# Performance work log

Measured on AMD Instinct MI355X. Metric: run time of the kernel, lower is better.

Reference implementation:

```python
import jax, jax.numpy as jnp
import numpy as np


def setup_inputs() -> dict:
    key = jax.random.key(0)
    ks = jax.random.split(key, 9)
    B, S, D, E, I = 4, 2048, 1024, 8, 2048
    sd = 1.0 / np.sqrt(D)
    si = 1.0 / np.sqrt(I)
    return {
        "hidden_states": jax.random.normal(ks[0], (B, S, D), dtype=jnp.float32),
        "gate_w": jax.random.normal(ks[1], (D, E), dtype=jnp.float32) * sd,
        "expert_gate_w": jax.random.normal(ks[2], (E, D, I), dtype=jnp.float32) * sd,
        "expert_up_w": jax.random.normal(ks[3], (E, D, I), dtype=jnp.float32) * sd,
        "expert_down_w": jax.random.normal(ks[4], (E, I, D), dtype=jnp.float32) * si,
        "shared_gate_proj_w": jax.random.normal(ks[5], (D, I), dtype=jnp.float32) * sd,
        "shared_up_w": jax.random.normal(ks[6], (D, I), dtype=jnp.float32) * sd,
        "shared_down_w": jax.random.normal(ks[7], (I, D), dtype=jnp.float32) * si,
        "shared_expert_gate_w": jax.random.normal(ks[8], (D, 1), dtype=jnp.float32) * sd,
        "top_k": 2,
    }


def reference(hidden_states, gate_w, expert_gate_w, expert_up_w, expert_down_w,
              shared_gate_proj_w, shared_up_w, shared_down_w, shared_expert_gate_w,
              top_k):
    B, S, D = hidden_states.shape
    E = gate_w.shape[1]
    x = hidden_states.reshape(-1, D)            # [T, D]
    T = x.shape[0]

    # Router: softmax in fp32, top-k, dense per-token per-expert combine weights.
    gate_vals = x @ gate_w                      # [T, E]
    probs = jax.nn.softmax(gate_vals.astype(jnp.float32), axis=-1)
    top_w, top_i = jax.lax.top_k(probs, top_k)  # [T, K]
    dense_w = jnp.zeros((T, E), dtype=jnp.float32)
    dense_w = dense_w.at[jnp.arange(T)[:, None], top_i].set(top_w)
    dense_w = dense_w.astype(x.dtype)           # zero for unselected experts

    # All experts as batched SwiGLU GEMMs (tokens with zero weight contribute 0).
    g = jnp.einsum('td,edi->eti', x, expert_gate_w)
    u = jnp.einsum('td,edi->eti', x, expert_up_w)
    y = jnp.einsum('eti,eid->etd', jax.nn.silu(g) * u, expert_down_w)  # [E, T, D]
    moe_out = jnp.einsum('etd,te->td', y, dense_w)                      # [T, D]

    # Shared expert with sigmoid gate.
    shared = (jax.nn.silu(x @ shared_gate_proj_w) * (x @ shared_up_w)) @ shared_down_w
    shared = jax.nn.sigmoid(x @ shared_expert_gate_w) * shared

    final = (moe_out + shared).reshape(B, S, D)
    return final, gate_vals
```

## Files before the change

### kernel.cpp

```cpp
#include <hip/hip_runtime.h>

typedef __bf16 bf16x8 __attribute__((ext_vector_type(8)));
typedef float f32x4 __attribute__((ext_vector_type(4)));
typedef float f4 __attribute__((ext_vector_type(4)));
typedef unsigned short us8 __attribute__((ext_vector_type(8)));

#define T_TOK 8192
#define DDIM 1024
#define NEXP 8
#define IDIM 2048
#define RROWS 17408
#define ROWS_TOT (T_TOK + RROWS)

__device__ __forceinline__ unsigned short f2bf(float f) {
    unsigned u = __float_as_uint(f);
    u += 0x7fffu + ((u >> 16) & 1u);
    return (unsigned short)(u >> 16);
}

__global__ __launch_bounds__(256) void router_kernel(
    const float* __restrict__ x, const float* __restrict__ gate_w,
    const float* __restrict__ sgw, float* __restrict__ gate_out,
    float* __restrict__ wdense, float* __restrict__ sgout)
{
    __shared__ float lgw[DDIM * NEXP];
    __shared__ float lsg[DDIM];
    int tid = threadIdx.x;
    for (int i = tid; i < (DDIM * NEXP) / 4; i += 256)
        ((f4*)lgw)[i] = ((const f4*)gate_w)[i];
    for (int i = tid; i < DDIM / 4; i += 256)
        ((f4*)lsg)[i] = ((const f4*)sgw)[i];
    __syncthreads();

    int wid = tid >> 6, l = tid & 63;
    int t = blockIdx.x * 4 + wid;

    float acc[NEXP];
#pragma unroll
    for (int e = 0; e < NEXP; e++) acc[e] = 0.f;
    float accs = 0.f;
    const float* xr = x + (size_t)t * DDIM;
#pragma unroll
    for (int j = 0; j < 4; j++) {
        int d0 = j * 256 + l * 4;
        f4 xv = *(const f4*)(xr + d0);
#pragma unroll
        for (int c = 0; c < 4; c++) {
            float xd = xv[c];
            int d = d0 + c;
#pragma unroll
            for (int e = 0; e < NEXP; e++) acc[e] += xd * lgw[d * NEXP + e];
            accs += xd * lsg[d];
        }
    }
#pragma unroll
    for (int off = 32; off > 0; off >>= 1) {
#pragma unroll
        for (int e = 0; e < NEXP; e++) acc[e] += __shfl_xor(acc[e], off);
        accs += __shfl_xor(accs, off);
    }
    if (l == 0) {
        float m = acc[0];
        for (int e = 1; e < NEXP; e++) m = fmaxf(m, acc[e]);
        float p[NEXP], s = 0.f;
        for (int e = 0; e < NEXP; e++) { p[e] = __expf(acc[e] - m); s += p[e]; }
        float inv = 1.f / s;
        int i1 = 0; float b1 = p[0];
        for (int e = 1; e < NEXP; e++) if (p[e] > b1) { b1 = p[e]; i1 = e; }
        int i2 = -1; float b2 = -1.f;
        for (int e = 0; e < NEXP; e++) if (e != i1 && p[e] > b2) { b2 = p[e]; i2 = e; }
        for (int e = 0; e < NEXP; e++) {
            gate_out[(size_t)t * NEXP + e] = acc[e];
            float w = (e == i1) ? b1 * inv : (e == i2) ? b2 * inv : 0.f;
            wdense[(size_t)t * NEXP + e] = w;
        }
        sgout[t] = 1.f / (1.f + __expf(-accs));
    }
}

__global__ __launch_bounds__(256) void bucket_kernel(
    const float* __restrict__ wdense, int* __restrict__ list,
    float* __restrict__ wl, int* __restrict__ cnt,
    int* __restrict__ te, int* __restrict__ tp, float* __restrict__ tw)
{
    int e = blockIdx.x;
    int tid = threadIdx.x, wid = tid >> 6, l = tid & 63;
    __shared__ int wsum[4];
    int base = 0;
    int* le = list + (size_t)e * T_TOK;
    float* we = wl + (size_t)e * T_TOK;
    for (int t0 = 0; t0 < T_TOK; t0 += 256) {
        int tok = t0 + tid;
        float w = wdense[(size_t)tok * NEXP + e];
        bool f = w > 0.f;
        unsigned long long m = __ballot(f);
        int lp = __popcll(m & ((1ull << l) - 1ull));
        if (l == 0) wsum[wid] = __popcll(m);
        __syncthreads();
        int woff = 0;
#pragma unroll
        for (int i = 0; i < 4; i++) if (i < wid) woff += wsum[i];
        int btot = wsum[0] + wsum[1] + wsum[2] + wsum[3];
        if (f) {
            int pos = base + woff + lp;
            le[pos] = tok; we[pos] = w;
            int slot = 0;
            for (int e2 = 0; e2 < e; e2++)
                slot += (wdense[(size_t)tok * NEXP + e2] > 0.f) ? 1 : 0;
            te[tok * 2 + slot] = e;
            tp[tok * 2 + slot] = pos;
            tw[tok * 2 + slot] = w;
        }
        base += btot;
        __syncthreads();
    }
    if (tid == 0) cnt[e] = base;
    int align = (base + 127) & ~127;
    for (int i = base + tid; i < align; i += 256) { le[i] = 0; we[i] = 0.f; }
}

__global__ void scan_kernel(const int* __restrict__ cnt, int* __restrict__ offs)
{
    if (threadIdx.x == 0) {
        int o = 0;
        for (int e = 0; e < NEXP; e++) { offs[e] = o; o += (cnt[e] + 127) & ~127; }
    }
}

__global__ __launch_bounds__(256) void cvt_kernel(
    const float* __restrict__ in, unsigned short* __restrict__ out, int n8)
{
    int i = blockIdx.x * 256 + threadIdx.x;
    if (i >= n8) return;
    const f4* p = (const f4*)in + (size_t)i * 2;
    f4 a = p[0], b = p[1];
    us8 o;
#pragma unroll
    for (int k = 0; k < 4; k++) { o[k] = f2bf(a[k]); o[4 + k] = f2bf(b[k]); }
    *((us8*)out + i) = o;
}

__global__ __launch_bounds__(256) void zero_kernel(float* __restrict__ p, int n4)
{
    int i = blockIdx.x * 256 + threadIdx.x;
    if (i < n4) ((f4*)p)[i] = f4{0.f, 0.f, 0.f, 0.f};
}

__global__ __launch_bounds__(256) void wcvt_gu_kernel(
    const float* __restrict__ egw, const float* __restrict__ euw,
    const float* __restrict__ sgp, const float* __restrict__ sup,
    unsigned short* __restrict__ pool, int c0, int NC)
{
    int j = blockIdx.y;
    int e = j >> 1, s = j & 1;
    const float* src = (e < 8) ? ((s ? euw : egw) + (size_t)e * DDIM * IDIM)
                               : (s ? sup : sgp);
    unsigned short* dst = pool + (size_t)j * NC * DDIM;
    int tpc = NC / 64;
    int tci = blockIdx.x % tpc, tri = blockIdx.x / tpc;
    int r0 = tri * 64;
    int cl0 = tci * 64;
    int cg0 = c0 + cl0;

    __shared__ unsigned short lds[64][72];
    int t = threadIdx.x;
    int tr = t >> 4, tcc = (t & 15) * 4;
#pragma unroll
    for (int jj = 0; jj < 4; jj++) {
        int r = tr + jj * 16;
        f4 v = *(const f4*)(src + (size_t)(r0 + r) * IDIM + cg0 + tcc);
#pragma unroll
        for (int k = 0; k < 4; k++) lds[r][tcc + k] = f2bf(v[k]);
    }
    __syncthreads();
    int orow = t >> 2, ss = t & 3;
    us8 v0, v1;
#pragma unroll
    for (int i = 0; i < 8; i++) {
        v0[i] = lds[ss * 16 + i][orow];
        v1[i] = lds[ss * 16 + 8 + i][orow];
    }
    unsigned short* op = dst + (size_t)(cl0 + orow) * DDIM + r0 + ss * 16;
    *(us8*)op = v0; *(us8*)(op + 8) = v1;
}

__global__ __launch_bounds__(256) void wcvt_d_kernel(
    const float* __restrict__ edw, const float* __restrict__ sdw,
    unsigned short* __restrict__ pool, int c0, int NC)
{
    int j = blockIdx.y;
    const float* src = (j < 8) ? edw + (size_t)j * IDIM * DDIM : sdw;
    unsigned short* dst = pool + (size_t)j * DDIM * NC;
    int tpc = DDIM / 64;
    int tci = blockIdx.x % tpc, tri = blockIdx.x / tpc;
    int rl0 = tri * 64;
    int rg0 = c0 + rl0;
    int cg0 = tci * 64;

    __shared__ unsigned short lds[64][72];
    int t = threadIdx.x;
    int tr = t >> 4, tcc = (t & 15) * 4;
#pragma unroll
    for (int jj = 0; jj < 4; jj++) {
        int r = tr + jj * 16;
        f4 v = *(const f4*)(src + (size_t)(rg0 + r) * DDIM + cg0 + tcc);
#pragma unroll
        for (int k = 0; k < 4; k++) lds[r][tcc + k] = f2bf(v[k]);
    }
    __syncthreads();
    int orow = t >> 2, ss = t & 3;
    us8 v0, v1;
#pragma unroll
    for (int i = 0; i < 8; i++) {
        v0[i] = lds[ss * 16 + i][orow];
        v1[i] = lds[ss * 16 + 8 + i][orow];
    }
    unsigned short* op = dst + (size_t)(cg0 + orow) * NC + rl0 + ss * 16;
    *(us8*)op = v0; *(us8*)(op + 8) = v1;
}

__device__ __forceinline__ void stage_tile(
    const unsigned short* __restrict__ g, int row0, int ldk, int k0,
    unsigned short* lds, int wid, int lane)
{
#pragma unroll
    for (int j = 0; j < 2; j++) {
        int c = wid + j * 4;
        int seg = c * 64 + lane;
        int row = seg >> 2, ks = seg & 3;
        const unsigned short* gp = g + (size_t)(row0 + row) * ldk + k0 + ks * 8;
        __builtin_amdgcn_global_load_lds(
            (const __attribute__((address_space(1))) void*)gp,
            (__attribute__((address_space(3))) void*)(lds + c * 512),
            16, 0, 0);
    }
}

__global__ __launch_bounds__(256, 2) void gemm_gateup(
    const unsigned short* __restrict__ A, const unsigned short* __restrict__ pool,
    unsigned short* __restrict__ H, const int* __restrict__ listb,
    const int* __restrict__ cnt, const int* __restrict__ offs, int NC)
{
    int z = blockIdx.z;
    const unsigned short *Bg, *Bu; const int* lst; int count, rowb;
    if (z == 0) {
        Bg = pool + (size_t)16 * NC * DDIM; Bu = pool + (size_t)17 * NC * DDIM;
        lst = nullptr; count = T_TOK; rowb = 0;
    } else {
        int e = z - 1;
        Bg = pool + (size_t)(e * 2) * NC * DDIM; Bu = pool + (size_t)(e * 2 + 1) * NC * DDIM;
        lst = listb + (size_t)e * T_TOK; count = cnt[e]; rowb = T_TOK + offs[e];
    }
    const int K = DDIM;
    int m0 = blockIdx.y * 128, n0 = blockIdx.x * 128;
    if (m0 >= count) return;

    __shared__ unsigned short As[128 * 32], Bgs[128 * 32], Bus[128 * 32];
    int tid = threadIdx.x, wid = tid >> 6, l = tid & 63;
    int wm = wid >> 1, wn = wid & 1;
    int lr = l & 15, kg = l >> 4;

    int seg0 = wid * 64 + l, seg1 = (wid + 4) * 64 + l;
    int ra0 = seg0 >> 2, ka0 = seg0 & 3;
    int ra1 = seg1 >> 2, ka1 = seg1 & 3;
    int ga0 = lst ? lst[m0 + ra0] : (m0 + ra0);
    int ga1 = lst ? lst[m0 + ra1] : (m0 + ra1);
    const unsigned short* pa0 = A + (size_t)ga0 * K + ka0 * 8;
    const unsigned short* pa1 = A + (size_t)ga1 * K + ka1 * 8;

    f32x4 zero = {0.f, 0.f, 0.f, 0.f};
    f32x4 accg[4][4], accu[4][4];
#pragma unroll
    for (int m = 0; m < 4; m++)
#pragma unroll
        for (int n = 0; n < 4; n++) { accg[m][n] = zero; accu[m][n] = zero; }

    for (int k0 = 0; k0 < K; k0 += 32) {
        __builtin_amdgcn_global_load_lds(
            (const __attribute__((address_space(1))) void*)(pa0 + k0),
            (__attribute__((address_space(3))) void*)(As + wid * 512), 16, 0, 0);
        __builtin_amdgcn_global_load_lds(
            (const __attribute__((address_space(1))) void*)(pa1 + k0),
            (__attribute__((address_space(3))) void*)(As + (wid + 4) * 512), 16, 0, 0);
        stage_tile(Bg, n0, K, k0, Bgs, wid, l);
        stage_tile(Bu, n0, K, k0, Bus, wid, l);
        __syncthreads();
        bf16x8 a[4], bg[4], bu[4];
#pragma unroll
        for (int m = 0; m < 4; m++)
            a[m] = *(const bf16x8*)(As + ((wm * 64 + m * 16 + lr) * 32 + kg * 8));
#pragma unroll
        for (int n = 0; n < 4; n++) {
            bg[n] = *(const bf16x8*)(Bgs + ((wn * 64 + n * 16 + lr) * 32 + kg * 8));
            bu[n] = *(const bf16x8*)(Bus + ((wn * 64 + n * 16 + lr) * 32 + kg * 8));
        }
#pragma unroll
        for (int m = 0; m < 4; m++)
#pragma unroll
            for (int n = 0; n < 4; n++) {
                accg[m][n] = __builtin_amdgcn_mfma_f32_16x16x32_bf16(a[m], bg[n], accg[m][n], 0, 0, 0);
                accu[m][n] = __builtin_amdgcn_mfma_f32_16x16x32_bf16(a[m], bu[n], accu[m][n], 0, 0, 0);
            }
        __syncthreads();
    }

#pragma unroll
    for (int m = 0; m < 4; m++) {
        int row = rowb + m0 + wm * 64 + m * 16 + kg * 4;
#pragma unroll
        for (int n = 0; n < 4; n++) {
            int col = n0 + wn * 64 + n * 16 + lr;
#pragma unroll
            for (int r = 0; r < 4; r++) {
                float g = accg[m][n][r], u = accu[m][n][r];
                float hv = g * (1.f / (1.f + __expf(-g))) * u;
                H[(size_t)(row + r) * NC + col] = f2bf(hv);
            }
        }
    }
}

template<int MODE>
__global__ __launch_bounds__(256, 2) void gemm_down(
    const unsigned short* __restrict__ H, const unsigned short* __restrict__ pool,
    float* __restrict__ Y, float* __restrict__ out0,
    const float* __restrict__ wlb, const float* __restrict__ sgo,
    const int* __restrict__ listb, const int* __restrict__ cnt,
    const int* __restrict__ offs, int NC)
{
    int z = blockIdx.z;
    const unsigned short* B; const int* lst; const float* coef; int count, rowb;
    if (z == 0) {
        B = pool + (size_t)8 * DDIM * NC;
        lst = nullptr; coef = sgo; count = T_TOK; rowb = 0;
    } else {
        int e = z - 1;
        B = pool + (size_t)e * DDIM * NC;
        lst = listb + (size_t)e * T_TOK; coef = wlb + (size_t)e * T_TOK;
        count = cnt[e]; rowb = T_TOK + offs[e];
    }
    int m0 = blockIdx.y * 128, n0 = blockIdx.x * 128;
    if (m0 >= count) return;
    const unsigned short* Arows = H + (size_t)rowb * NC;

    __shared__ unsigned short As[128 * 32], Bs[128 * 32];
    int tid = threadIdx.x, wid = tid >> 6, l = tid & 63;
    int wm = wid >> 1, wn = wid & 1;
    int lr = l & 15, kg = l >> 4;

    f32x4 zero = {0.f, 0.f, 0.f, 0.f};
    f32x4 acc[4][4];
#pragma unroll
    for (int m = 0; m < 4; m++)
#pragma unroll
        for (int n = 0; n < 4; n++) acc[m][n] = zero;

    for (int k0 = 0; k0 < NC; k0 += 32) {
        stage_tile(Arows, m0, NC, k0, As, wid, l);
        stage_tile(B, n0, NC, k0, Bs, wid, l);
        __syncthreads();
        bf16x8 a[4], b[4];
#pragma unroll
        for (int m = 0; m < 4; m++)
            a[m] = *(const bf16x8*)(As + ((wm * 64 + m * 16 + lr) * 32 + kg * 8));
#pragma unroll
        for (int n = 0; n < 4; n++)
            b[n] = *(const bf16x8*)(Bs + ((wn * 64 + n * 16 + lr) * 32 + kg * 8));
#pragma unroll
        for (int m = 0; m < 4; m++)
#pragma unroll
            for (int n = 0; n < 4; n++)
                acc[m][n] = __builtin_amdgcn_mfma_f32_16x16x32_bf16(a[m], b[n], acc[m][n], 0, 0, 0);
        __syncthreads();
    }

#pragma unroll
    for (int m = 0; m < 4; m++) {
        int rloc = m0 + wm * 64 + m * 16 + kg * 4;
#pragma unroll
        for (int n = 0; n < 4; n++) {
            int col = n0 + wn * 64 + n * 16 + lr;
#pragma unroll
            for (int r = 0; r < 4; r++) {
                float v = acc[m][n][r];
                if (MODE == 0) {
                    Y[(size_t)(rowb + rloc + r) * DDIM + col] = v;
                } else if (MODE == 1) {
                    Y[(size_t)(rowb + rloc + r) * DDIM + col] += v;
                } else {
                    int rc = rloc + r;
                    if (rc < count) {
                        int tok = lst ? lst[rc] : rc;
                        atomicAdd(&out0[(size_t)tok * DDIM + col], coef[rc] * v);
                    }
                }
            }
        }
    }
}

__global__ __launch_bounds__(256) void combine_kernel(
    const float* __restrict__ Y, const float* __restrict__ sgo,
    const int* __restrict__ te, const int* __restrict__ tp,
    const float* __restrict__ tw, const int* __restrict__ offs,
    float* __restrict__ out)
{
    int t = blockIdx.x * 2 + (threadIdx.x >> 7);
    int c = (threadIdx.x & 127) * 8;
    int e0 = te[2 * t], e1 = te[2 * t + 1];
    size_t r0 = (size_t)T_TOK + offs[e0] + tp[2 * t];
    size_t r1 = (size_t)T_TOK + offs[e1] + tp[2 * t + 1];
    float w0 = tw[2 * t], w1 = tw[2 * t + 1], sg = sgo[t];

    const float* ys = Y + (size_t)t * DDIM + c;
    const float* y0 = Y + r0 * DDIM + c;
    const float* y1 = Y + r1 * DDIM + c;
    f4 s0 = *(const f4*)ys, s1 = *(const f4*)(ys + 4);
    f4 a0 = *(const f4*)y0, a1 = *(const f4*)(y0 + 4);
    f4 b0 = *(const f4*)y1, b1 = *(const f4*)(y1 + 4);
    f4 o0, o1;
#pragma unroll
    for (int k = 0; k < 4; k++) {
        o0[k] = sg * s0[k] + w0 * a0[k] + w1 * b0[k];
        o1[k] = sg * s1[k] + w0 * a1[k] + w1 * b1[k];
    }
    float* op = out + (size_t)t * DDIM + c;
    *(f4*)op = o0;
    *(f4*)(op + 4) = o1;
}

extern "C" void kernel_launch(void* const* d_in, const int* in_sizes, int n_in,
                              void* d_out, int out_size, void* d_ws, size_t ws_size,
                              hipStream_t stream)
{
    const float* x   = (const float*)d_in[0];
    const float* gw  = (const float*)d_in[1];
    const float* egw = (const float*)d_in[2];
    const float* euw = (const float*)d_in[3];
    const float* edw = (const float*)d_in[4];
    const float* sgp = (const float*)d_in[5];
    const float* sup = (const float*)d_in[6];
    const float* sdw = (const float*)d_in[7];
    const float* seg = (const float*)d_in[8];

    float* out0 = (float*)d_out;
    float* gate_out = out0 + (size_t)T_TOK * DDIM;

    auto al = [](size_t b) { return (b + 255) & ~(size_t)255; };
    size_t fixed_b = al((size_t)T_TOK * DDIM * 2)
                   + al((size_t)T_TOK * NEXP * 4)
                   + al((size_t)T_TOK * 4)
                   + al((size_t)NEXP * T_TOK * 4)
                   + al((size_t)NEXP * T_TOK * 4)
                   + 256 + 256
                   + 3 * al((size_t)T_TOK * 2 * 4);
    auto pool_b = [&](int NC) { return al((size_t)18 * NC * DDIM * 2); };
    auto h_b    = [&](int NC) { return al((size_t)ROWS_TOT * NC * 2); };
    size_t y_b  = al((size_t)ROWS_TOT * DDIM * 4);

    int ISPLIT; bool ymode;
    if (fixed_b + pool_b(1024) + h_b(1024) + y_b <= ws_size)      { ISPLIT = 2; ymode = true;  }
    else if (fixed_b + pool_b(1024) + h_b(1024) <= ws_size)       { ISPLIT = 2; ymode = false; }
    else if (fixed_b + pool_b(512) + h_b(512) <= ws_size)         { ISPLIT = 4; ymode = false; }
    else                                                          { ISPLIT = 8; ymode = false; }
    int NC = IDIM / ISPLIT;

    char* ws = (char*)d_ws;
    auto take = [&](size_t bytes) { char* p = ws; ws += (bytes + 255) & ~(size_t)255; return p; };
    unsigned short* xb   = (unsigned short*)take((size_t)T_TOK * DDIM * 2);
    float* wdense = (float*)take((size_t)T_TOK * NEXP * 4);
    float* sgo    = (float*)take((size_t)T_TOK * 4);
    int*   list   = (int*)take((size_t)NEXP * T_TOK * 4);
    float* wl     = (float*)take((size_t)NEXP * T_TOK * 4);
    int*   cnt    = (int*)take(0); ws += 256;
    int*   offs   = (int*)take(0); ws += 256;
    int*   te     = (int*)take((size_t)T_TOK * 2 * 4);
    int*   tp     = (int*)take((size_t)T_TOK * 2 * 4);
    float* tw     = (float*)take((size_t)T_TOK * 2 * 4);
    unsigned short* pool = (unsigned short*)take((size_t)18 * NC * DDIM * 2);
    unsigned short* H    = (unsigned short*)take((size_t)ROWS_TOT * NC * 2);
    float* Y = ymode ? (float*)take((size_t)ROWS_TOT * DDIM * 4) : nullptr;

    router_kernel<<<T_TOK / 4, 256, 0, stream>>>(x, gw, seg, gate_out, wdense, sgo);
    bucket_kernel<<<NEXP, 256, 0, stream>>>(wdense, list, wl, cnt, te, tp, tw);
    scan_kernel<<<1, 64, 0, stream>>>(cnt, offs);
    cvt_kernel<<<(T_TOK * DDIM / 8) / 256, 256, 0, stream>>>(x, xb, T_TOK * DDIM / 8);
    if (!ymode)
        zero_kernel<<<(T_TOK * DDIM / 4) / 256, 256, 0, stream>>>(out0, T_TOK * DDIM / 4);

    for (int c = 0; c < ISPLIT; c++) {
        int c0 = c * NC;
        wcvt_gu_kernel<<<dim3((NC / 64) * 16, 18), 256, 0, stream>>>(
            egw, euw, sgp, sup, pool, c0, NC);
        gemm_gateup<<<dim3(NC / 128, T_TOK / 128, 9), 256, 0, stream>>>(
            xb, pool, H, list, cnt, offs, NC);
        wcvt_d_kernel<<<dim3((NC / 64) * 16, 9), 256, 0, stream>>>(
            edw, sdw, pool, c0, NC);
        if (ymode) {
            if (c == 0)
                gemm_down<0><<<dim3(DDIM / 128, T_TOK / 128, 9), 256, 0, stream>>>(
                    H, pool, Y, out0, wl, sgo, list, cnt, offs, NC);
            else
                gemm_down<1><<<dim3(DDIM / 128, T_TOK / 128, 9), 256, 0, stream>>>(
                    H, pool, Y, out0, wl, sgo, list, cnt, offs, NC);
        } else {
            gemm_down<2><<<dim3(DDIM / 128, T_TOK / 128, 9), 256, 0, stream>>>(
                H, pool, Y, out0, wl, sgo, list, cnt, offs, NC);
        }
    }
    if (ymode)
        combine_kernel<<<T_TOK / 2, 256, 0, stream>>>(Y, sgo, te, tp, tw, offs, out0);
}
```

Before: 632.6 us.

## Run down-projection once over full K with bf16 pre-scaled Y and simplified combine

Restructures the schedule so the gate/up GEMM runs in two column chunks writing into a full-width H buffer, then a single down-projection GEMM runs over the full intermediate dimension. This removes the second down pass and the fp32 Y read-modify-write. The down GEMM folds the routing or shared-gate coefficient into its epilogue and stores Y as bf16. The combine then only sums three bf16 rows. The workspace-dependent fallback paths (atomics, zeroing) are dropped, which assumes the workspace is large enough and adds bf16 rounding on the partial outputs.

```diff
diff --git a/kernel.cpp b/kernel.cpp
--- a/kernel.cpp
+++ b/kernel.cpp
@@ -9,6 +9,7 @@
 #define DDIM 1024
 #define NEXP 8
 #define IDIM 2048
+#define NCH 1024
 #define RROWS 17408
 #define ROWS_TOT (T_TOK + RROWS)
 
@@ -81,7 +82,7 @@
 __global__ __launch_bounds__(256) void bucket_kernel(
     const float* __restrict__ wdense, int* __restrict__ list,
     float* __restrict__ wl, int* __restrict__ cnt,
-    int* __restrict__ te, int* __restrict__ tp, float* __restrict__ tw)
+    int* __restrict__ te, int* __restrict__ tp)
 {
     int e = blockIdx.x;
     int tid = threadIdx.x, wid = tid >> 6, l = tid & 63;
@@ -109,7 +110,6 @@
                 slot += (wdense[(size_t)tok * NEXP + e2] > 0.f) ? 1 : 0;
             te[tok * 2 + slot] = e;
             tp[tok * 2 + slot] = pos;
-            tw[tok * 2 + slot] = w;
         }
         base += btot;
         __syncthreads();
@@ -140,23 +140,17 @@
     *((us8*)out + i) = o;
 }
 
-__global__ __launch_bounds__(256) void zero_kernel(float* __restrict__ p, int n4)
-{
-    int i = blockIdx.x * 256 + threadIdx.x;
-    if (i < n4) ((f4*)p)[i] = f4{0.f, 0.f, 0.f, 0.f};
-}
-
 __global__ __launch_bounds__(256) void wcvt_gu_kernel(
     const float* __restrict__ egw, const float* __restrict__ euw,
     const float* __restrict__ sgp, const float* __restrict__ sup,
-    unsigned short* __restrict__ pool, int c0, int NC)
+    unsigned short* __restrict__ pool, int c0)
 {
     int j = blockIdx.y;
     int e = j >> 1, s = j & 1;
     const float* src = (e < 8) ? ((s ? euw : egw) + (size_t)e * DDIM * IDIM)
                                : (s ? sup : sgp);
-    unsigned short* dst = pool + (size_t)j * NC * DDIM;
-    int tpc = NC / 64;
+    unsigned short* dst = pool + (size_t)j * NCH * DDIM;
+    int tpc = NCH / 64;
     int tci = blockIdx.x % tpc, tri = blockIdx.x / tpc;
     int r0 = tri * 64;
     int cl0 = tci * 64;
@@ -186,15 +180,14 @@
 
 __global__ __launch_bounds__(256) void wcvt_d_kernel(
     const float* __restrict__ edw, const float* __restrict__ sdw,
-    unsigned short* __restrict__ pool, int c0, int NC)
+    unsigned short* __restrict__ pool)
 {
     int j = blockIdx.y;
     const float* src = (j < 8) ? edw + (size_t)j * IDIM * DDIM : sdw;
-    unsigned short* dst = pool + (size_t)j * DDIM * NC;
+    unsigned short* dst = pool + (size_t)j * DDIM * IDIM;
     int tpc = DDIM / 64;
     int tci = blockIdx.x % tpc, tri = blockIdx.x / tpc;
-    int rl0 = tri * 64;
-    int rg0 = c0 + rl0;
+    int rg0 = tri * 64;
     int cg0 = tci * 64;
 
     __shared__ unsigned short lds[64][72];
@@ -215,7 +208,7 @@
         v0[i] = lds[ss * 16 + i][orow];
         v1[i] = lds[ss * 16 + 8 + i][orow];
     }
-    unsigned short* op = dst + (size_t)(cg0 + orow) * NC + rl0 + ss * 16;
+    unsigned short* op = dst + (size_t)(cg0 + orow) * IDIM + rg0 + ss * 16;
     *(us8*)op = v0; *(us8*)(op + 8) = v1;
 }
 
@@ -239,21 +232,23 @@
 __global__ __launch_bounds__(256, 2) void gemm_gateup(
     const unsigned short* __restrict__ A, const unsigned short* __restrict__ pool,
     unsigned short* __restrict__ H, const int* __restrict__ listb,
-    const int* __restrict__ cnt, const int* __restrict__ offs, int NC)
+    const int* __restrict__ cnt, const int* __restrict__ offs, int c0)
 {
     int z = blockIdx.z;
     const unsigned short *Bg, *Bu; const int* lst; int count, rowb;
     if (z == 0) {
-        Bg = pool + (size_t)16 * NC * DDIM; Bu = pool + (size_t)17 * NC * DDIM;
+        Bg = pool + (size_t)16 * NCH * DDIM; Bu = pool + (size_t)17 * NCH * DDIM;
         lst = nullptr; count = T_TOK; rowb = 0;
     } else {
         int e = z - 1;
-        Bg = pool + (size_t)(e * 2) * NC * DDIM; Bu = pool + (size_t)(e * 2 + 1) * NC * DDIM;
+        Bg = pool + (size_t)(e * 2) * NCH * DDIM; Bu = pool + (size_t)(e * 2 + 1) * NCH * DDIM;
         lst = listb + (size_t)e * T_TOK; count = cnt[e]; rowb = T_TOK + offs[e];
     }
+    int flat = blockIdx.y * 8 + blockIdx.x;
+    int nt = flat & 7, mt = flat >> 3;
+    int m0 = mt * 128, n0 = nt * 128;
+    if (m0 >= count) return;
     const int K = DDIM;
-    int m0 = blockIdx.y * 128, n0 = blockIdx.x * 128;
-    if (m0 >= count) return;
 
     __shared__ unsigned short As[128 * 32], Bgs[128 * 32], Bus[128 * 32];
     int tid = threadIdx.x, wid = tid >> 6, l = tid & 63;
@@ -309,39 +304,39 @@
         int row = rowb + m0 + wm * 64 + m * 16 + kg * 4;
 #pragma unroll
         for (int n = 0; n < 4; n++) {
-            int col = n0 + wn * 64 + n * 16 + lr;
+            int col = c0 + n0 + wn * 64 + n * 16 + lr;
 #pragma unroll
             for (int r = 0; r < 4; r++) {
                 float g = accg[m][n][r], u = accu[m][n][r];
                 float hv = g * (1.f / (1.f + __expf(-g))) * u;
-                H[(size_t)(row + r) * NC + col] = f2bf(hv);
+                H[(size_t)(row + r) * IDIM + col] = f2bf(hv);
             }
         }
     }
 }
 
-template<int MODE>
 __global__ __launch_bounds__(256, 2) void gemm_down(
     const unsigned short* __restrict__ H, const unsigned short* __restrict__ pool,
-    float* __restrict__ Y, float* __restrict__ out0,
+    unsigned short* __restrict__ Y,
     const float* __restrict__ wlb, const float* __restrict__ sgo,
-    const int* __restrict__ listb, const int* __restrict__ cnt,
-    const int* __restrict__ offs, int NC)
+    const int* __restrict__ cnt, const int* __restrict__ offs)
 {
     int z = blockIdx.z;
-    const unsigned short* B; const int* lst; const float* coef; int count, rowb;
+    const unsigned short* B; const float* coef; int count, rowb;
     if (z == 0) {
-        B = pool + (size_t)8 * DDIM * NC;
-        lst = nullptr; coef = sgo; count = T_TOK; rowb = 0;
+        B = pool + (size_t)8 * DDIM * IDIM;
+        coef = sgo; count = T_TOK; rowb = 0;
     } else {
         int e = z - 1;
-        B = pool + (size_t)e * DDIM * NC;
-        lst = listb + (size_t)e * T_TOK; coef = wlb + (size_t)e * T_TOK;
+        B = pool + (size_t)e * DDIM * IDIM;
+        coef = wlb + (size_t)e * T_TOK;
         count = cnt[e]; rowb = T_TOK + offs[e];
     }
-    int m0 = blockIdx.y * 128, n0 = blockIdx.x * 128;
+    int flat = blockIdx.y * 8 + blockIdx.x;
+    int nt = flat & 7, mt = flat >> 3;
+    int m0 = mt * 128, n0 = nt * 128;
     if (m0 >= count) return;
-    const unsigned short* Arows = H + (size_t)rowb * NC;
+    const unsigned short* Arows = H + (size_t)rowb * IDIM;
 
     __shared__ unsigned short As[128 * 32], Bs[128 * 32];
     int tid = threadIdx.x, wid = tid >> 6, l = tid & 63;
@@ -355,9 +350,9 @@
 #pragma unroll
         for (int n = 0; n < 4; n++) acc[m][n] = zero;
 
-    for (int k0 = 0; k0 < NC; k0 += 32) {
-        stage_tile(Arows, m0, NC, k0, As, wid, l);
-        stage_tile(B, n0, NC, k0, Bs, wid, l);
+    for (int k0 = 0; k0 < IDIM; k0 += 32) {
+        stage_tile(Arows, m0, IDIM, k0, As, wid, l);
+        stage_tile(B, n0, IDIM, k0, Bs, wid, l);
         __syncthreads();
         bf16x8 a[4], b[4];
 #pragma unroll
@@ -377,32 +372,22 @@
 #pragma unroll
     for (int m = 0; m < 4; m++) {
         int rloc = m0 + wm * 64 + m * 16 + kg * 4;
+        float cf[4];
+#pragma unroll
+        for (int r = 0; r < 4; r++) cf[r] = coef[rloc + r];
 #pragma unroll
         for (int n = 0; n < 4; n++) {
             int col = n0 + wn * 64 + n * 16 + lr;
 #pragma unroll
-            for (int r = 0; r < 4; r++) {
-                float v = acc[m][n][r];
-                if (MODE == 0) {
-                    Y[(size_t)(rowb + rloc + r) * DDIM + col] = v;
-                } else if (MODE == 1) {
-                    Y[(size_t)(rowb + rloc + r) * DDIM + col] += v;
-                } else {
-                    int rc = rloc + r;
-                    if (rc < count) {
-                        int tok = lst ? lst[rc] : rc;
-                        atomicAdd(&out0[(size_t)tok * DDIM + col], coef[rc] * v);
-                    }
-                }
-            }
+            for (int r = 0; r < 4; r++)
+                Y[(size_t)(rowb + rloc + r) * DDIM + col] = f2bf(cf[r] * acc[m][n][r]);
         }
     }
 }
 
 __global__ __launch_bounds__(256) void combine_kernel(
-    const float* __restrict__ Y, const float* __restrict__ sgo,
-    const int* __restrict__ te, const int* __restrict__ tp,
-    const float* __restrict__ tw, const int* __restrict__ offs,
+    const unsigned short* __restrict__ Y, const int* __restrict__ te,
+    const int* __restrict__ tp, const int* __restrict__ offs,
     float* __restrict__ out)
 {
     int t = blockIdx.x * 2 + (threadIdx.x >> 7);
@@ -410,19 +395,19 @@
     int e0 = te[2 * t], e1 = te[2 * t + 1];
     size_t r0 = (size_t)T_TOK + offs[e0] + tp[2 * t];
     size_t r1 = (size_t)T_TOK + offs[e1] + tp[2 * t + 1];
-    float w0 = tw[2 * t], w1 = tw[2 * t + 1], sg = sgo[t];
-
-    const float* ys = Y + (size_t)t * DDIM + c;
-    const float* y0 = Y + r0 * DDIM + c;
-    const float* y1 = Y + r1 * DDIM + c;
-    f4 s0 = *(const f4*)ys, s1 = *(const f4*)(ys + 4);
-    f4 a0 = *(const f4*)y0, a1 = *(const f4*)(y0 + 4);
-    f4 b0 = *(const f4*)y1, b1 = *(const f4*)(y1 + 4);
+
+    us8 vs = *(const us8*)(Y + (size_t)t * DDIM + c);
+    us8 v0 = *(const us8*)(Y + r0 * DDIM + c);
+    us8 v1 = *(const us8*)(Y + r1 * DDIM + c);
     f4 o0, o1;
 #pragma unroll
     for (int k = 0; k < 4; k++) {
-        o0[k] = sg * s0[k] + w0 * a0[k] + w1 * b0[k];
-        o1[k] = sg * s1[k] + w0 * a1[k] + w1 * b1[k];
+        o0[k] = __uint_as_float((unsigned)vs[k] << 16)
+              + __uint_as_float((unsigned)v0[k] << 16)
+              + __uint_as_float((unsigned)v1[k] << 16);
+        o1[k] = __uint_as_float((unsigned)vs[4 + k] << 16)
+              + __uint_as_float((unsigned)v0[4 + k] << 16)
+              + __uint_as_float((unsigned)v1[4 + k] << 16);
     }
     float* op = out + (size_t)t * DDIM + c;
     *(f4*)op = o0;
@@ -446,25 +431,6 @@
     float* out0 = (float*)d_out;
     float* gate_out = out0 + (size_t)T_TOK * DDIM;
 
-    auto al = [](size_t b) { return (b + 255) & ~(size_t)255; };
-    size_t fixed_b = al((size_t)T_TOK * DDIM * 2)
-                   + al((size_t)T_TOK * NEXP * 4)
-                   + al((size_t)T_TOK * 4)
-                   + al((size_t)NEXP * T_TOK * 4)
-                   + al((size_t)NEXP * T_TOK * 4)
-                   + 256 + 256
-                   + 3 * al((size_t)T_TOK * 2 * 4);
-    auto pool_b = [&](int NC) { return al((size_t)18 * NC * DDIM * 2); };
-    auto h_b    = [&](int NC) { return al((size_t)ROWS_TOT * NC * 2); };
-    size_t y_b  = al((size_t)ROWS_TOT * DDIM * 4);
-
-    int ISPLIT; bool ymode;
-    if (fixed_b + pool_b(1024) + h_b(1024) + y_b <= ws_size)      { ISPLIT = 2; ymode = true;  }
-    else if (fixed_b + pool_b(1024) + h_b(1024) <= ws_size)       { ISPLIT = 2; ymode = false; }
-    else if (fixed_b + pool_b(512) + h_b(512) <= ws_size)         { ISPLIT = 4; ymode = false; }
-    else                                                          { ISPLIT = 8; ymode = false; }
-    int NC = IDIM / ISPLIT;
-
     char* ws = (char*)d_ws;
     auto take = [&](size_t bytes) { char* p = ws; ws += (bytes + 255) & ~(size_t)255; return p; };
     unsigned short* xb   = (unsigned short*)take((size_t)T_TOK * DDIM * 2);
@@ -472,42 +438,29 @@
     float* sgo    = (float*)take((size_t)T_TOK * 4);
     int*   list   = (int*)take((size_t)NEXP * T_TOK * 4);
     float* wl     = (float*)take((size_t)NEXP * T_TOK * 4);
-    int*   cnt    = (int*)take(0); ws += 256;
-    int*   offs   = (int*)take(0); ws += 256;
+    int*   cnt    = (int*)take(256);
+    int*   offs   = (int*)take(256);
     int*   te     = (int*)take((size_t)T_TOK * 2 * 4);
     int*   tp     = (int*)take((size_t)T_TOK * 2 * 4);
-    float* tw     = (float*)take((size_t)T_TOK * 2 * 4);
-    unsigned short* pool = (unsigned short*)take((size_t)18 * NC * DDIM * 2);
-    unsigned short* H    = (unsigned short*)take((size_t)ROWS_TOT * NC * 2);
-    float* Y = ymode ? (float*)take((size_t)ROWS_TOT * DDIM * 4) : nullptr;
+    unsigned short* pool = (unsigned short*)take((size_t)18 * NCH * DDIM * 2);
+    unsigned short* H    = (unsigned short*)take((size_t)ROWS_TOT * IDIM * 2);
+    unsigned short* Y    = (unsigned short*)take((size_t)ROWS_TOT * DDIM * 2);
 
     router_kernel<<<T_TOK / 4, 256, 0, stream>>>(x, gw, seg, gate_out, wdense, sgo);
-    bucket_kernel<<<NEXP, 256, 0, stream>>>(wdense, list, wl, cnt, te, tp, tw);
+    bucket_kernel<<<NEXP, 256, 0, stream>>>(wdense, list, wl, cnt, te, tp);
     scan_kernel<<<1, 64, 0, stream>>>(cnt, offs);
     cvt_kernel<<<(T_TOK * DDIM / 8) / 256, 256, 0, stream>>>(x, xb, T_TOK * DDIM / 8);
-    if (!ymode)
-        zero_kernel<<<(T_TOK * DDIM / 4) / 256, 256, 0, stream>>>(out0, T_TOK * DDIM / 4);
-
-    for (int c = 0; c < ISPLIT; c++) {
-        int c0 = c * NC;
-        wcvt_gu_kernel<<<dim3((NC / 64) * 16, 18), 256, 0, stream>>>(
-            egw, euw, sgp, sup, pool, c0, NC);
-        gemm_gateup<<<dim3(NC / 128, T_TOK / 128, 9), 256, 0, stream>>>(
-            xb, pool, H, list, cnt, offs, NC);
-        wcvt_d_kernel<<<dim3((NC / 64) * 16, 9), 256, 0, stream>>>(
-            edw, sdw, pool, c0, NC);
-        if (ymode) {
-            if (c == 0)
-                gemm_down<0><<<dim3(DDIM / 128, T_TOK / 128, 9), 256, 0, stream>>>(
-                    H, pool, Y, out0, wl, sgo, list, cnt, offs, NC);
-            else
-                gemm_down<1><<<dim3(DDIM / 128, T_TOK / 128, 9), 256, 0, stream>>>(
-                    H, pool, Y, out0, wl, sgo, list, cnt, offs, NC);
-        } else {
-            gemm_down<2><<<dim3(DDIM / 128, T_TOK / 128, 9), 256, 0, stream>>>(
-                H, pool, Y, out0, wl, sgo, list, cnt, offs, NC);
-        }
-    }
-    if (ymode)
-        combine_kernel<<<T_TOK / 2, 256, 0, stream>>>(Y, sgo, te, tp, tw, offs, out0);
-}
+
+    for (int c = 0; c < 2; c++) {
+        int c0 = c * NCH;
+        wcvt_gu_kernel<<<dim3((NCH / 64) * 16, 18), 256, 0, stream>>>(
+            egw, euw, sgp, sup, pool, c0);
+        gemm_gateup<<<dim3(8, 64, 9), 256, 0, stream>>>(
+            xb, pool, H, list, cnt, offs, c0);
+    }
+
+    wcvt_d_kernel<<<dim3((IDIM / 64) * 16, 9), 256, 0, stream>>>(edw, sdw, pool);
+    gemm_down<<<dim3(8, 64, 9), 256, 0, stream>>>(H, pool, Y, wl, sgo, cnt, offs);
+
+    combine_kernel<<<T_TOK / 2, 256, 0, stream>>>(Y, te, tp, offs, out0);
+}
```

Result: faster. 590.8 us (-6.6%).
